# Performance work log

Hardware: AMD Instinct MI355X
Metric: run time of the kernel (lower is better)

The kernel has to match this reference:

```python
import jax, jax.numpy as jnp
import numpy as np

INPUT_DIM = 1024
HIDDEN = 64
NUM_MEM = 8   # +1 shared slot -> 9 total
K = 2
SEQ = 256
BATCH = 32


def setup_inputs() -> dict:
    key = jax.random.key(0)
    ks = jax.random.split(key, 10)
    s = 1.0 / np.sqrt(INPUT_DIM)
    nm1 = NUM_MEM + 1
    return {
        "X": jax.random.normal(ks[0], (SEQ, BATCH, INPUT_DIM), jnp.float32),
        "M_0": jnp.zeros((BATCH, nm1, HIDDEN, HIDDEN), jnp.float32),
        "Wk_w": jax.random.uniform(ks[1], (HIDDEN * nm1, INPUT_DIM), jnp.float32, -s, s),
        "Wk_b": jax.random.uniform(ks[2], (HIDDEN * nm1,), jnp.float32, -s, s),
        "Wv_w": jax.random.uniform(ks[3], (HIDDEN * nm1, INPUT_DIM), jnp.float32, -s, s),
        "Wv_b": jax.random.uniform(ks[4], (HIDDEN * nm1,), jnp.float32, -s, s),
        "Wg_w": jax.random.uniform(ks[5], (NUM_MEM, INPUT_DIM), jnp.float32, -s, s),
        "Wg_b": jax.random.uniform(ks[6], (NUM_MEM,), jnp.float32, -s, s),
        "Wq_w": jax.random.uniform(ks[7], (HIDDEN, INPUT_DIM), jnp.float32, -s, s),
        "Wq_b": jax.random.uniform(ks[8], (HIDDEN,), jnp.float32, -s, s),
    }


def _mom_forward(X, M_0, Wk_w, Wk_b, Wv_w, Wv_b, Wg_w, Wg_b, Wq_w, Wq_b):
    B = X.shape[1]
    nm1 = NUM_MEM + 1
    b_idx = jnp.arange(B)[:, None]

    def step(M, x_t):
        # gating + top-k routing (sorted descending, like torch.topk)
        score = jax.nn.softmax(x_t @ Wg_w.T + Wg_b, axis=1)          # (B, NUM_MEM)
        m_scores, m_idx = jax.lax.top_k(score, K)                    # (B, K)
        idx_update = jnp.concatenate(
            [jnp.zeros((B, 1), jnp.int32), m_idx.astype(jnp.int32)], axis=1)  # (B, K+1)
        g = m_scores / jnp.sum(m_scores, axis=1, keepdims=True)     # (B, K)

        Mk = (x_t @ Wk_w.T + Wk_b).reshape(B, nm1, HIDDEN)          # (B, 9, H)
        Mv = (x_t @ Wv_w.T + Wv_b).reshape(B, nm1, HIDDEN)
        # only gather the K+1 routed outer products instead of all 9
        k_sel = jnp.take_along_axis(Mk, idx_update[:, :, None], axis=1)  # (B, K+1, H)
        v_sel = jnp.take_along_axis(Mv, idx_update[:, :, None], axis=1)
        src = k_sel[..., :, None] * v_sel[..., None, :]              # (B, K+1, H, H)
        M = M.at[b_idx, idx_update].add(src)                         # scatter-add (dupes accumulate)

        M_use = M[b_idx, m_idx]                                      # (B, K, H, H)
        M_out = jnp.einsum('bk,bkij->bij', g, M_use) + M[:, 0]       # add shared memory
        q = x_t @ Wq_w.T + Wq_b                                      # (B, H)
        o = jnp.einsum('bi,bij->bj', q, M_out)                       # (B, H)
        return M, o

    M_final, outputs = jax.lax.scan(step, M_0, X)
    return outputs, M_final


def reference(X, M_0, Wk_w, Wk_b, Wv_w, Wv_b, Wg_w, Wg_b, Wq_w, Wq_b):
    return _mom_forward(X, M_0, Wk_w, Wk_b, Wv_w, Wv_b, Wg_w, Wg_b, Wq_w, Wq_b)
```

## Files before the change

kernel.cpp:

```cpp
#include <hip/hip_runtime.h>
#include <stdint.h>

#define SEQ 256
#define BATCH 32
#define IN_DIM 1024
#define HID 64
#define NPAD 1280
#define ROWS (SEQ*BATCH)

#define XBF_OFF   0
#define DMH_OFF   0
#define WBF_OFF   16777216
#define BB_OFF    19398656
#define GATE_OFF  19403776
#define Y_OFF     19534848

#define NC 8
#define CHL 32

#define DM_CB_U32 18432

typedef __attribute__((ext_vector_type(8))) short short8;
typedef __attribute__((ext_vector_type(4))) float floatx4;

typedef const __attribute__((address_space(1))) unsigned int gas_u32;
typedef __attribute__((address_space(3))) unsigned int las_u32;
static __device__ __forceinline__ void gl_lds16(const void* g, void* l) {
  __builtin_amdgcn_global_load_lds((gas_u32*)g, (las_u32*)l, 16, 0, 0);
}

static __device__ __forceinline__ short f2bf(float f) {
  union { float f; uint32_t u; } a; a.f = f;
  uint32_t r = (a.u + 0x7FFFu + ((a.u >> 16) & 1u)) >> 16;
  return (short)r;
}
static __device__ __forceinline__ float bflo(uint32_t u){ return __uint_as_float(u << 16); }
static __device__ __forceinline__ float bfhi(uint32_t u){ return __uint_as_float(u & 0xffff0000u); }
static __device__ __forceinline__ float bfu(unsigned short us){ return __uint_as_float(((uint32_t)us) << 16); }

__global__ __launch_bounds__(256) void prep_gate_kernel(
    const float* __restrict__ X,
    const float* __restrict__ Wk, const float* __restrict__ bk,
    const float* __restrict__ Wv, const float* __restrict__ bv,
    const float* __restrict__ Wg, const float* __restrict__ bg,
    const float* __restrict__ Wq, const float* __restrict__ bq,
    short* __restrict__ Xbf, short* __restrict__ Wbf,
    float* __restrict__ bb, float4* __restrict__ gate)
{
  if (blockIdx.x < 2048) {
    int64_t idx = (int64_t)blockIdx.x * blockDim.x + threadIdx.x;
    int64_t stride = (int64_t)2048 * 256;
    const int64_t NX4 = (int64_t)ROWS * IN_DIM / 4;
    for (int64_t i = idx; i < NX4; i += stride) {
      float4 x = ((const float4*)X)[i];
      short4 s4;
      s4.x = f2bf(x.x); s4.y = f2bf(x.y); s4.z = f2bf(x.z); s4.w = f2bf(x.w);
      ((short4*)Xbf)[i] = s4;
    }
    const int64_t NW4 = (int64_t)NPAD * IN_DIM / 4;
    for (int64_t i = idx; i < NW4; i += stride) {
      int64_t e = i * 4;
      int r = (int)(e >> 10);
      int k = (int)(e & 1023);
      float4 x;
      if (r < 576)       x = *(const float4*)(Wk + (int64_t)r*1024 + k);
      else if (r < 1152) x = *(const float4*)(Wv + (int64_t)(r-576)*1024 + k);
      else if (r < 1216) x = *(const float4*)(Wq + (int64_t)(r-1152)*1024 + k);
      else               x = make_float4(0.f, 0.f, 0.f, 0.f);
      short4 s4;
      s4.x = f2bf(x.x); s4.y = f2bf(x.y); s4.z = f2bf(x.z); s4.w = f2bf(x.w);
      ((short4*)Wbf)[i] = s4;
    }
    for (int64_t i = idx; i < NPAD; i += stride) {
      int r = (int)i; float v;
      if (r < 576)       v = bk[r];
      else if (r < 1152) v = bv[r - 576];
      else if (r < 1216) v = bq[r - 1152];
      else               v = 0.f;
      bb[r] = v;
    }
  } else {
    const int lane = threadIdx.x & 63;
    const int row  = (blockIdx.x - 2048) * 4 + (threadIdx.x >> 6);
    const float* x = X + (int64_t)row * IN_DIM;

    float acc[8];
#pragma unroll
    for (int e = 0; e < 8; e++) acc[e] = 0.f;
#pragma unroll
    for (int i = 0; i < 4; i++) {
      const int off = i * 256 + lane * 4;
      float4 xv = *(const float4*)(x + off);
#pragma unroll
      for (int e = 0; e < 8; e++) {
        float4 wv = *(const float4*)(Wg + e * IN_DIM + off);
        acc[e] += xv.x * wv.x + xv.y * wv.y + xv.z * wv.z + xv.w * wv.w;
      }
    }
#pragma unroll
    for (int e = 0; e < 8; e++) {
#pragma unroll
      for (int m = 32; m >= 1; m >>= 1)
        acc[e] += __shfl_xor(acc[e], m);
      acc[e] += bg[e];
    }
    if (lane == 0) {
      int i0 = 0; float v0 = acc[0];
#pragma unroll
      for (int e = 1; e < 8; e++) if (acc[e] > v0) { v0 = acc[e]; i0 = e; }
      int i1 = -1; float v1 = -3.4e38f;
#pragma unroll
      for (int e = 0; e < 8; e++) if (e != i0 && acc[e] > v1) { v1 = acc[e]; i1 = e; }
      float e1 = __expf(v1 - v0);
      float inv = 1.f / (1.f + e1);
      gate[row] = make_float4(__int_as_float(i0), __int_as_float(i1), inv, e1 * inv);
    }
  }
}

__global__ __launch_bounds__(256) void gemm_kernel(
    const short* __restrict__ Xbf,
    const short* __restrict__ Wbf,
    const float* __restrict__ bb,
    float* __restrict__ Y)
{
  __shared__ short As[128 * 32];
  __shared__ short Bs[128 * 32];

  const int tid  = threadIdx.x;
  const int lane = tid & 63;
  const int wv   = tid >> 6;
  const int quad = lane >> 4;
  const int cl   = lane & 15;
  const int wm   = wv & 1;
  const int wn   = wv >> 1;
  const int m0 = blockIdx.y * 128;
  const int n0 = blockIdx.x * 128;

  const int srow = wv * 32 + (lane >> 2);
  const int scol = (lane & 3) * 8;
  const short* gA = Xbf + (int64_t)(m0 + srow) * IN_DIM + scol;
  const short* gB = Wbf + (int64_t)(n0 + srow) * IN_DIM + scol;
  short* lA = As + (wv * 32) * 32;
  short* lB = Bs + (wv * 32) * 32;

  floatx4 acc[4][4];
#pragma unroll
  for (int i = 0; i < 4; i++)
#pragma unroll
    for (int k = 0; k < 4; k++) acc[i][k] = (floatx4){0.f, 0.f, 0.f, 0.f};

  for (int ks = 0; ks < IN_DIM; ks += 32) {
    gl_lds16(gA + ks,                lA);
    gl_lds16(gA + 16 * IN_DIM + ks,  lA + 16 * 32);
    gl_lds16(gB + ks,                lB);
    gl_lds16(gB + 16 * IN_DIM + ks,  lB + 16 * 32);
    __syncthreads();

    short8 bfrag[4], afrag[4];
#pragma unroll
    for (int nt = 0; nt < 4; nt++)
      bfrag[nt] = *(const short8*)(&Bs[(wn * 64 + nt * 16 + cl) * 32 + quad * 8]);
#pragma unroll
    for (int mt = 0; mt < 4; mt++)
      afrag[mt] = *(const short8*)(&As[(wm * 64 + mt * 16 + cl) * 32 + quad * 8]);
#pragma unroll
    for (int mt = 0; mt < 4; mt++)
#pragma unroll
      for (int nt = 0; nt < 4; nt++)
        acc[mt][nt] = __builtin_amdgcn_mfma_f32_16x16x32_bf16(afrag[mt], bfrag[nt], acc[mt][nt], 0, 0, 0);
    __syncthreads();
  }

#pragma unroll
  for (int nt = 0; nt < 4; nt++) {
    const int col = n0 + wn * 64 + nt * 16 + cl;
    const float bias = bb[col];
#pragma unroll
    for (int mt = 0; mt < 4; mt++) {
#pragma unroll
      for (int r = 0; r < 4; r++) {
        int row = m0 + wm * 64 + mt * 16 + quad * 4 + r;
        Y[(int64_t)row * NPAD + col] = acc[mt][nt][r] + bias;
      }
    }
  }
}

__global__ __launch_bounds__(256) void mfma_chunk_kernel(
    const float* __restrict__ Y, const float4* __restrict__ gate,
    unsigned short* __restrict__ DMu, float* __restrict__ out)
{
  __shared__ uint32_t Qs[32 * 32];
  __shared__ uint32_t Ks[96 * 32];
  __shared__ unsigned short Kts[64 * 104];
  __shared__ unsigned short Vts[64 * 104];
  __shared__ unsigned short Ps[32 * 104];
  __shared__ float4 gl[32];
  __shared__ uint32_t su[96];

  const int blk = blockIdx.x;
  const int c   = blk & 7;
  const int b   = blk >> 3;
  const int tid = threadIdx.x;
  const int lane = tid & 63;
  const int wv  = tid >> 6;
  const int quad = lane >> 4;
  const int cl  = lane & 15;
  const int t0  = c * CHL;

  if (tid < 32) {
    float4 g = gate[(t0 + tid) * BATCH + b];
    gl[tid] = g;
    su[3 * tid]     = 0u;
    su[3 * tid + 1] = (uint32_t)__float_as_int(g.x);
    su[3 * tid + 2] = (uint32_t)__float_as_int(g.y);
  }
  __syncthreads();

  for (int idx = tid; idx < 3072; idx += 256) {
    const int e = idx >> 5, dd = idx & 31;
    const int s = (e * 171) >> 9;
    const int u = e - 3 * s;
    const int head = (u == 0) ? 0 : (int)su[3 * s + u];
    const float* Yr = Y + ((int64_t)(t0 + s) * BATCH + b) * NPAD;
    float f0 = Yr[head * 64 + 2 * dd], f1 = Yr[head * 64 + 2 * dd + 1];
    unsigned short b0 = (unsigned short)f2bf(f0), b1 = (unsigned short)f2bf(f1);
    Ks[e * 32 + dd] = (uint32_t)b0 | ((uint32_t)b1 << 16);
    Kts[(2 * dd) * 104 + e] = b0;
    Kts[(2 * dd + 1) * 104 + e] = b1;
    float v0 = Yr[576 + head * 64 + 2 * dd], v1 = Yr[576 + head * 64 + 2 * dd + 1];
    Vts[(2 * dd) * 104 + e] = (unsigned short)f2bf(v0);
    Vts[(2 * dd + 1) * 104 + e] = (unsigned short)f2bf(v1);
  }
  for (int idx = tid; idx < 1024; idx += 256) {
    const int s = idx >> 5, dd = idx & 31;
    const float* Yr = Y + ((int64_t)(t0 + s) * BATCH + b) * NPAD;
    Qs[s * 32 + dd] = ((uint32_t)(unsigned short)f2bf(Yr[1152 + 2 * dd])) |
                      (((uint32_t)(unsigned short)f2bf(Yr[1152 + 2 * dd + 1])) << 16);
  }
  __syncthreads();

  const unsigned short* Qu = (const unsigned short*)Qs;
  const unsigned short* Ku = (const unsigned short*)Ks;

#pragma unroll
  for (int q3 = 0; q3 < 3; q3++) {
    const int tileId = wv * 3 + q3;
    const int mt = tileId / 6, nt = tileId % 6;
    floatx4 acc = (floatx4){0.f, 0.f, 0.f, 0.f};
#pragma unroll
    for (int kc = 0; kc < 2; kc++) {
      short8 af = *(const short8*)(Qu + (mt * 16 + cl) * 64 + kc * 32 + quad * 8);
      short8 bf = *(const short8*)(Ku + (nt * 16 + cl) * 64 + kc * 32 + quad * 8);
      acc = __builtin_amdgcn_mfma_f32_16x16x32_bf16(af, bf, acc, 0, 0, 0);
    }
    const int e = nt * 16 + cl;
    const int s_e = (e * 171) >> 9;
    const int slot_e = (int)su[e];
#pragma unroll
    for (int r = 0; r < 4; r++) {
      const int t = mt * 16 + quad * 4 + r;
      float4 g = gl[t];
      const int i0t = __float_as_int(g.x), i1t = __float_as_int(g.y);
      float w = (slot_e == 0 ? 1.f : 0.f)
              + (slot_e == i0t ? g.z : 0.f)
              + (slot_e == i1t ? g.w : 0.f);
      w = (s_e <= t) ? w : 0.f;
      Ps[t * 104 + e] = (unsigned short)f2bf(w * acc[r]);
    }
  }
  __syncthreads();

#pragma unroll
  for (int q2 = 0; q2 < 2; q2++) {
    const int tileId = wv + q2 * 4;
    const int mt = tileId >> 2, nt = tileId & 3;
    floatx4 acc = (floatx4){0.f, 0.f, 0.f, 0.f};
#pragma unroll
    for (int kc = 0; kc < 3; kc++) {
      short8 af = *(const short8*)(Ps  + (mt * 16 + cl) * 104 + kc * 32 + quad * 8);
      short8 bf = *(const short8*)(Vts + (nt * 16 + cl) * 104 + kc * 32 + quad * 8);
      acc = __builtin_amdgcn_mfma_f32_16x16x32_bf16(af, bf, acc, 0, 0, 0);
    }
#pragma unroll
    for (int r = 0; r < 4; r++) {
      const int t = mt * 16 + quad * 4 + r, j = nt * 16 + cl;
      out[(int64_t)(t0 + t) * (BATCH * HID) + b * HID + j] = acc[r];
    }
  }

  uint32_t sreg[3][8];
#pragma unroll
  for (int kc = 0; kc < 3; kc++)
#pragma unroll
    for (int jj = 0; jj < 8; jj++)
      sreg[kc][jj] = su[kc * 32 + quad * 8 + jj];

  short8 afc[4][3];
#pragma unroll
  for (int mt = 0; mt < 4; mt++)
#pragma unroll
    for (int kc = 0; kc < 3; kc++)
      afc[mt][kc] = *(const short8*)(Kts + (mt * 16 + cl) * 104 + kc * 32 + quad * 8);

  unsigned short* dmb = DMu + ((int64_t)(c * 32 + b)) * 36864;
  union U8 { short8 s; uint32_t u[4]; };

  for (int mi = wv; mi < 9; mi += 4) {
    uint32_t md[3][4];
#pragma unroll
    for (int kc = 0; kc < 3; kc++)
#pragma unroll
      for (int p = 0; p < 4; p++)
        md[kc][p] = ((sreg[kc][2 * p]     == (uint32_t)mi) ? 0x0000ffffu : 0u) |
                    ((sreg[kc][2 * p + 1] == (uint32_t)mi) ? 0xffff0000u : 0u);
#pragma unroll
    for (int nt = 0; nt < 4; nt++) {
      short8 bm[3];
#pragma unroll
      for (int kc = 0; kc < 3; kc++) {
        U8 vv; vv.s = *(const short8*)(Vts + (nt * 16 + cl) * 104 + kc * 32 + quad * 8);
        vv.u[0] &= md[kc][0]; vv.u[1] &= md[kc][1];
        vv.u[2] &= md[kc][2]; vv.u[3] &= md[kc][3];
        bm[kc] = vv.s;
      }
#pragma unroll
      for (int mt = 0; mt < 4; mt++) {
        floatx4 acc = (floatx4){0.f, 0.f, 0.f, 0.f};
#pragma unroll
        for (int kc = 0; kc < 3; kc++)
          acc = __builtin_amdgcn_mfma_f32_16x16x32_bf16(afc[mt][kc], bm[kc], acc, 0, 0, 0);
#pragma unroll
        for (int r = 0; r < 4; r++) {
          const int i = mt * 16 + quad * 4 + r, j = nt * 16 + cl;
          dmb[mi * 4096 + i * 64 + j] = (unsigned short)f2bf(acc[r]);
        }
      }
    }
  }
}

__global__ void prefix_kernel(const float* __restrict__ M0, uint32_t* __restrict__ DMh,
                              float* __restrict__ out, int nc)
{
  int64_t e = (int64_t)blockIdx.x * blockDim.x + threadIdx.x;
  int b = (int)(e / DM_CB_U32);
  int r = (int)(e % DM_CB_U32);
  int m = r >> 11, rem = r & 2047, i = rem >> 5, jp = rem & 31;
  int64_t f32i = (int64_t)b * 36864 + m * 4096 + i * 64 + jp * 2;
  float run0 = M0[f32i], run1 = M0[f32i + 1];
  for (int cc = 0; cc < nc; cc++) {
    int64_t idx = ((int64_t)(cc * 32 + b)) * DM_CB_U32 + r;
    uint32_t u = DMh[idx];
    DMh[idx] = ((uint32_t)(unsigned short)f2bf(run0)) |
               (((uint32_t)(unsigned short)f2bf(run1)) << 16);
    run0 += bflo(u); run1 += bfhi(u);
  }
  *(float2*)(out + (int64_t)SEQ * BATCH * HID + f32i) = make_float2(run0, run1);
}

__global__ __launch_bounds__(256) void corr_kernel(
    const float* __restrict__ Y, const float4* __restrict__ gate,
    const uint32_t* __restrict__ DMh, float* __restrict__ out)
{
  __shared__ uint32_t Msb32[9 * 64 * 16];
  __shared__ float2 qb[32 * 32];
  __shared__ float4 gl[32];
  unsigned short* Msb = (unsigned short*)Msb32;
  const int blk = blockIdx.x;
  const int c   = blk & 7;
  const int jh  = (blk >> 3) & 1;
  const int b   = blk >> 4;
  const int tid = threadIdx.x;
  const int t0  = c * CHL;

  if (tid < 32) gl[tid] = gate[(t0 + tid) * BATCH + b];
#pragma unroll
  for (int k = 0; k < 4; k++) {
    int f = tid + 256 * k;
    int t = f >> 5, p = f & 31;
    qb[t * 32 + p] = *(const float2*)(Y + ((int64_t)(t0 + t) * BATCH + b) * NPAD + 1152 + 2 * p);
  }
  const uint32_t* dmb = DMh + ((int64_t)(c * 32 + b)) * DM_CB_U32;
#pragma unroll
  for (int k = 0; k < 36; k++) {
    int f = tid + 256 * k;
    int m = f >> 10, rem = f & 1023, i = rem >> 4, p = rem & 15;
    Msb32[(m * 64 + i) * 16 + p] = dmb[m * 2048 + i * 32 + jh * 16 + p];
  }
  __syncthreads();

  const int jj = tid & 31;
  const int tg = tid >> 5;
#pragma unroll
  for (int tt = 0; tt < 4; tt++) {
    const int t = tt * 8 + tg;
    float4 g = gl[t];
    const int i0 = __float_as_int(g.x), i1 = __float_as_int(g.y);
    const float g0 = g.z, g1 = g.w;
    float acc = 0.f;
#pragma unroll 8
    for (int i2 = 0; i2 < 32; i2++) {
      float2 qq = qb[t * 32 + i2];
      int ia = 2 * i2;
      float m0a = bfu(Msb[(0  * 64 + ia) * 32 + jj]);
      float m0b = bfu(Msb[(0  * 64 + ia + 1) * 32 + jj]);
      float maa = bfu(Msb[(i0 * 64 + ia) * 32 + jj]);
      float mab = bfu(Msb[(i0 * 64 + ia + 1) * 32 + jj]);
      float mba = bfu(Msb[(i1 * 64 + ia) * 32 + jj]);
      float mbb = bfu(Msb[(i1 * 64 + ia + 1) * 32 + jj]);
      acc += qq.x * (m0a + g0 * maa + g1 * mba);
      acc += qq.y * (m0b + g0 * mab + g1 * mbb);
    }
    float* op = out + (int64_t)(t0 + t) * (BATCH * HID) + b * HID + jh * 32 + jj;
    *op += acc;
  }
}

extern "C" void kernel_launch(void* const* d_in, const int* in_sizes, int n_in,
                              void* d_out, int out_size, void* d_ws, size_t ws_size,
                              hipStream_t stream)
{
  const float* X  = (const float*)d_in[0];
  const float* M0 = (const float*)d_in[1];
  const float* Wk = (const float*)d_in[2];
  const float* bk = (const float*)d_in[3];
  const float* Wv = (const float*)d_in[4];
  const float* bv = (const float*)d_in[5];
  const float* Wg = (const float*)d_in[6];
  const float* bg = (const float*)d_in[7];
  const float* Wq = (const float*)d_in[8];
  const float* bq = (const float*)d_in[9];

  char* ws = (char*)d_ws;
  short*          Xbf  = (short*)(ws + XBF_OFF);
  short*          Wbf  = (short*)(ws + WBF_OFF);
  float*          bb   = (float*)(ws + BB_OFF);
  float4*         gate = (float4*)(ws + GATE_OFF);
  float*          Y    = (float*)(ws + Y_OFF);
  uint32_t*       DMh  = (uint32_t*)(ws + DMH_OFF);
  unsigned short* DMu  = (unsigned short*)(ws + DMH_OFF);
  float*          out  = (float*)d_out;

  prep_gate_kernel<<<4096, 256, 0, stream>>>(X, Wk, bk, Wv, bv, Wg, bg, Wq, bq,
                                             Xbf, Wbf, bb, gate);
  dim3 gg(NPAD / 128, ROWS / 128);
  gemm_kernel<<<gg, 256, 0, stream>>>(Xbf, Wbf, bb, Y);
  mfma_chunk_kernel<<<32 * NC, 256, 0, stream>>>(Y, gate, DMu, out);
  prefix_kernel<<<(32 * DM_CB_U32) / 256, 256, 0, stream>>>(M0, DMh, out, NC);
  corr_kernel<<<32 * NC * 2, 256, 0, stream>>>(Y, gate, DMh, out);
}
```

Baseline: 182.2 us.

## Widen chunk kernel to 512 threads, vectorize loads, transpose corr smem, batch prefix loads

The chunk kernel now runs with 512 threads (8 waves). Its Y reads use float4 loads and the tile loops are redistributed across the extra waves. The prefix kernel loads all NC chunk deltas up front to expose memory-level parallelism. The corr kernel stores M transposed in shared memory so each thread reads contiguous bf16 pairs with 64-bit loads. Doubling threads in the chunk kernel leaves some waves idle in the 9-memory and 12-tile loops, and the transposed shared stores may cause bank conflicts.

```diff
diff --git a/kernel.cpp b/kernel.cpp
--- a/kernel.cpp
+++ b/kernel.cpp
@@ -187,7 +187,7 @@
   }
 }
 
-__global__ __launch_bounds__(256) void mfma_chunk_kernel(
+__global__ __launch_bounds__(512) void mfma_chunk_kernel(
     const float* __restrict__ Y, const float4* __restrict__ gate,
     unsigned short* __restrict__ DMu, float* __restrict__ out)
 {
@@ -218,35 +218,43 @@
   }
   __syncthreads();
 
-  for (int idx = tid; idx < 3072; idx += 256) {
-    const int e = idx >> 5, dd = idx & 31;
+  for (int idx = tid; idx < 1536; idx += 512) {
+    const int e = idx >> 4, d4 = idx & 15;
     const int s = (e * 171) >> 9;
     const int u = e - 3 * s;
     const int head = (u == 0) ? 0 : (int)su[3 * s + u];
     const float* Yr = Y + ((int64_t)(t0 + s) * BATCH + b) * NPAD;
-    float f0 = Yr[head * 64 + 2 * dd], f1 = Yr[head * 64 + 2 * dd + 1];
-    unsigned short b0 = (unsigned short)f2bf(f0), b1 = (unsigned short)f2bf(f1);
-    Ks[e * 32 + dd] = (uint32_t)b0 | ((uint32_t)b1 << 16);
-    Kts[(2 * dd) * 104 + e] = b0;
-    Kts[(2 * dd + 1) * 104 + e] = b1;
-    float v0 = Yr[576 + head * 64 + 2 * dd], v1 = Yr[576 + head * 64 + 2 * dd + 1];
-    Vts[(2 * dd) * 104 + e] = (unsigned short)f2bf(v0);
-    Vts[(2 * dd + 1) * 104 + e] = (unsigned short)f2bf(v1);
-  }
-  for (int idx = tid; idx < 1024; idx += 256) {
-    const int s = idx >> 5, dd = idx & 31;
+    float4 kf = *(const float4*)(Yr + head * 64 + 4 * d4);
+    unsigned short k0 = (unsigned short)f2bf(kf.x), k1 = (unsigned short)f2bf(kf.y);
+    unsigned short k2 = (unsigned short)f2bf(kf.z), k3 = (unsigned short)f2bf(kf.w);
+    uint2 kp; kp.x = (uint32_t)k0 | ((uint32_t)k1 << 16);
+    kp.y = (uint32_t)k2 | ((uint32_t)k3 << 16);
+    *(uint2*)&Ks[e * 32 + 2 * d4] = kp;
+    Kts[(4 * d4)     * 104 + e] = k0;
+    Kts[(4 * d4 + 1) * 104 + e] = k1;
+    Kts[(4 * d4 + 2) * 104 + e] = k2;
+    Kts[(4 * d4 + 3) * 104 + e] = k3;
+    float4 vf = *(const float4*)(Yr + 576 + head * 64 + 4 * d4);
+    Vts[(4 * d4)     * 104 + e] = (unsigned short)f2bf(vf.x);
+    Vts[(4 * d4 + 1) * 104 + e] = (unsigned short)f2bf(vf.y);
+    Vts[(4 * d4 + 2) * 104 + e] = (unsigned short)f2bf(vf.z);
+    Vts[(4 * d4 + 3) * 104 + e] = (unsigned short)f2bf(vf.w);
+  }
+  {
+    const int s = tid >> 4, d4 = tid & 15;
     const float* Yr = Y + ((int64_t)(t0 + s) * BATCH + b) * NPAD;
-    Qs[s * 32 + dd] = ((uint32_t)(unsigned short)f2bf(Yr[1152 + 2 * dd])) |
-                      (((uint32_t)(unsigned short)f2bf(Yr[1152 + 2 * dd + 1])) << 16);
+    float4 qf = *(const float4*)(Yr + 1152 + 4 * d4);
+    uint2 qp;
+    qp.x = (uint32_t)(unsigned short)f2bf(qf.x) | (((uint32_t)(unsigned short)f2bf(qf.y)) << 16);
+    qp.y = (uint32_t)(unsigned short)f2bf(qf.z) | (((uint32_t)(unsigned short)f2bf(qf.w)) << 16);
+    *(uint2*)&Qs[s * 32 + 2 * d4] = qp;
   }
   __syncthreads();
 
   const unsigned short* Qu = (const unsigned short*)Qs;
   const unsigned short* Ku = (const unsigned short*)Ks;
 
-#pragma unroll
-  for (int q3 = 0; q3 < 3; q3++) {
-    const int tileId = wv * 3 + q3;
+  for (int tileId = wv; tileId < 12; tileId += 8) {
     const int mt = tileId / 6, nt = tileId % 6;
     floatx4 acc = (floatx4){0.f, 0.f, 0.f, 0.f};
 #pragma unroll
@@ -272,9 +280,8 @@
   }
   __syncthreads();
 
-#pragma unroll
-  for (int q2 = 0; q2 < 2; q2++) {
-    const int tileId = wv + q2 * 4;
+  {
+    const int tileId = wv;
     const int mt = tileId >> 2, nt = tileId & 3;
     floatx4 acc = (floatx4){0.f, 0.f, 0.f, 0.f};
 #pragma unroll
@@ -307,7 +314,7 @@
   unsigned short* dmb = DMu + ((int64_t)(c * 32 + b)) * 36864;
   union U8 { short8 s; uint32_t u[4]; };
 
-  for (int mi = wv; mi < 9; mi += 4) {
+  for (int mi = wv; mi < 9; mi += 8) {
     uint32_t md[3][4];
 #pragma unroll
     for (int kc = 0; kc < 3; kc++)
@@ -342,7 +349,7 @@
 }
 
 __global__ void prefix_kernel(const float* __restrict__ M0, uint32_t* __restrict__ DMh,
-                              float* __restrict__ out, int nc)
+                              float* __restrict__ out)
 {
   int64_t e = (int64_t)blockIdx.x * blockDim.x + threadIdx.x;
   int b = (int)(e / DM_CB_U32);
@@ -350,12 +357,16 @@
   int m = r >> 11, rem = r & 2047, i = rem >> 5, jp = rem & 31;
   int64_t f32i = (int64_t)b * 36864 + m * 4096 + i * 64 + jp * 2;
   float run0 = M0[f32i], run1 = M0[f32i + 1];
-  for (int cc = 0; cc < nc; cc++) {
+  uint32_t u[NC];
+#pragma unroll
+  for (int cc = 0; cc < NC; cc++)
+    u[cc] = DMh[((int64_t)(cc * 32 + b)) * DM_CB_U32 + r];
+#pragma unroll
+  for (int cc = 0; cc < NC; cc++) {
     int64_t idx = ((int64_t)(cc * 32 + b)) * DM_CB_U32 + r;
-    uint32_t u = DMh[idx];
     DMh[idx] = ((uint32_t)(unsigned short)f2bf(run0)) |
                (((uint32_t)(unsigned short)f2bf(run1)) << 16);
-    run0 += bflo(u); run1 += bfhi(u);
+    run0 += bflo(u[cc]); run1 += bfhi(u[cc]);
   }
   *(float2*)(out + (int64_t)SEQ * BATCH * HID + f32i) = make_float2(run0, run1);
 }
@@ -364,10 +375,9 @@
     const float* __restrict__ Y, const float4* __restrict__ gate,
     const uint32_t* __restrict__ DMh, float* __restrict__ out)
 {
-  __shared__ uint32_t Msb32[9 * 64 * 16];
+  __shared__ unsigned short MsbT[9 * 32 * 68];
   __shared__ float2 qb[32 * 32];
   __shared__ float4 gl[32];
-  unsigned short* Msb = (unsigned short*)Msb32;
   const int blk = blockIdx.x;
   const int c   = blk & 7;
   const int jh  = (blk >> 3) & 1;
@@ -387,7 +397,9 @@
   for (int k = 0; k < 36; k++) {
     int f = tid + 256 * k;
     int m = f >> 10, rem = f & 1023, i = rem >> 4, p = rem & 15;
-    Msb32[(m * 64 + i) * 16 + p] = dmb[m * 2048 + i * 32 + jh * 16 + p];
+    uint32_t u = dmb[m * 2048 + i * 32 + jh * 16 + p];
+    MsbT[(m * 32 + 2 * p)     * 68 + i] = (unsigned short)(u & 0xffffu);
+    MsbT[(m * 32 + 2 * p + 1) * 68 + i] = (unsigned short)(u >> 16);
   }
   __syncthreads();
 
@@ -399,19 +411,21 @@
     float4 g = gl[t];
     const int i0 = __float_as_int(g.x), i1 = __float_as_int(g.y);
     const float g0 = g.z, g1 = g.w;
+    const unsigned short* P0 = MsbT + (0  * 32 + jj) * 68;
+    const unsigned short* Pa = MsbT + (i0 * 32 + jj) * 68;
+    const unsigned short* Pb = MsbT + (i1 * 32 + jj) * 68;
     float acc = 0.f;
-#pragma unroll 8
-    for (int i2 = 0; i2 < 32; i2++) {
-      float2 qq = qb[t * 32 + i2];
-      int ia = 2 * i2;
-      float m0a = bfu(Msb[(0  * 64 + ia) * 32 + jj]);
-      float m0b = bfu(Msb[(0  * 64 + ia + 1) * 32 + jj]);
-      float maa = bfu(Msb[(i0 * 64 + ia) * 32 + jj]);
-      float mab = bfu(Msb[(i0 * 64 + ia + 1) * 32 + jj]);
-      float mba = bfu(Msb[(i1 * 64 + ia) * 32 + jj]);
-      float mbb = bfu(Msb[(i1 * 64 + ia + 1) * 32 + jj]);
-      acc += qq.x * (m0a + g0 * maa + g1 * mba);
-      acc += qq.y * (m0b + g0 * mab + g1 * mbb);
+#pragma unroll 4
+    for (int i4 = 0; i4 < 16; i4++) {
+      float2 qq0 = qb[t * 32 + 2 * i4];
+      float2 qq1 = qb[t * 32 + 2 * i4 + 1];
+      uint2 a0 = *(const uint2*)(P0 + 4 * i4);
+      uint2 aa = *(const uint2*)(Pa + 4 * i4);
+      uint2 ab = *(const uint2*)(Pb + 4 * i4);
+      acc += qq0.x * (bflo(a0.x) + g0 * bflo(aa.x) + g1 * bflo(ab.x));
+      acc += qq0.y * (bfhi(a0.x) + g0 * bfhi(aa.x) + g1 * bfhi(ab.x));
+      acc += qq1.x * (bflo(a0.y) + g0 * bflo(aa.y) + g1 * bflo(ab.y));
+      acc += qq1.y * (bfhi(a0.y) + g0 * bfhi(aa.y) + g1 * bfhi(ab.y));
     }
     float* op = out + (int64_t)(t0 + t) * (BATCH * HID) + b * HID + jh * 32 + jj;
     *op += acc;
@@ -447,7 +461,7 @@
                                              Xbf, Wbf, bb, gate);
   dim3 gg(NPAD / 128, ROWS / 128);
   gemm_kernel<<<gg, 256, 0, stream>>>(Xbf, Wbf, bb, Y);
-  mfma_chunk_kernel<<<32 * NC, 256, 0, stream>>>(Y, gate, DMu, out);
-  prefix_kernel<<<(32 * DM_CB_U32) / 256, 256, 0, stream>>>(M0, DMh, out, NC);
+  mfma_chunk_kernel<<<32 * NC, 512, 0, stream>>>(Y, gate, DMu, out);
+  prefix_kernel<<<(32 * DM_CB_U32) / 256, 256, 0, stream>>>(M0, DMh, out);
   corr_kernel<<<32 * NC * 2, 256, 0, stream>>>(Y, gate, DMh, out);
 }
```

After: 173.8 us. 1.05x faster.
